# Optimization experiments

Hardware: AMD Instinct MI355X
Metric: run time of the kernel (lower is better)

The kernel has to match this reference:

```python
import jax, jax.numpy as jnp
import numpy as np

B, T, C = 64, 256, 384
H, D = 6, 64  # num_heads, head_size

def setup_inputs() -> dict:
    key = jax.random.key(0)
    ks = jax.random.split(key, 6)
    s = 0.02
    return {
        "x": jax.random.normal(ks[0], (B, T, C), dtype=jnp.float32),
        "Wq": jax.random.normal(ks[1], (H, C, D), dtype=jnp.float32) * s,
        "Wk": jax.random.normal(ks[2], (H, C, D), dtype=jnp.float32) * s,
        "Wv": jax.random.normal(ks[3], (H, C, D), dtype=jnp.float32) * s,
        "Wp": jax.random.normal(ks[4], (C, C), dtype=jnp.float32) * s,
        "bp": jnp.zeros((C,), dtype=jnp.float32),
    }

def reference(x, Wq, Wk, Wv, Wp, bp):
    # per-head projections: [B,T,C] x [H,C,D] -> [B,H,T,D]
    q = jnp.einsum('btc,hcd->bhtd', x, Wq)
    k = jnp.einsum('btc,hcd->bhtd', x, Wk)
    v = jnp.einsum('btc,hcd->bhtd', x, Wv)
    scale = 1.0 / jnp.sqrt(jnp.float32(D))
    scores = jnp.einsum('bhtd,bhsd->bhts', q, k) * scale  # [B,H,T,T]
    Tlen = x.shape[1]
    causal = jnp.tril(jnp.ones((Tlen, Tlen), dtype=bool))
    scores = jnp.where(causal, scores, -jnp.inf)
    wei = jax.nn.softmax(scores, axis=-1)
    # dropout is identity in eval mode
    out = jnp.einsum('bhts,bhsd->bhtd', wei, v)  # [B,H,T,D]
    # concat heads in order (matches torch.cat over head list)
    out = jnp.transpose(out, (0, 2, 1, 3)).reshape(x.shape[0], Tlen, H * D)
    return out @ Wp.T + bp  # nn.Linear: y = x W^T + b
```

## Files before the change

kernel.cpp:

```cpp
#include <hip/hip_runtime.h>

constexpr int Bn = 64, T = 256, C = 384, H = 6, D = 64;
constexpr int BT = Bn * T;
constexpr int NQKV = 3 * C;
constexpr int WALL_ELEMS = NQKV * C;
constexpr int WP_ELEMS = C * C;

using f32x4 = __attribute__((ext_vector_type(4))) float;
using fvec4 = __attribute__((ext_vector_type(4))) float;
using us8   = __attribute__((ext_vector_type(8))) unsigned short;
using bf8   = __attribute__((ext_vector_type(8))) __bf16;

__device__ __forceinline__ unsigned short f2bf(float f) {
  unsigned u = __builtin_bit_cast(unsigned, f);
  u += 0x7FFFu + ((u >> 16) & 1u);
  return (unsigned short)(u >> 16);
}

__device__ __forceinline__ f32x4 mfma16(us8 a, us8 b, f32x4 c) {
  return __builtin_amdgcn_mfma_f32_16x16x32_bf16(
      __builtin_bit_cast(bf8, a), __builtin_bit_cast(bf8, b), c, 0, 0, 0);
}

__global__ __launch_bounds__(256) void k_prep(
    const float* __restrict__ Wq, const float* __restrict__ Wk,
    const float* __restrict__ Wv, const float* __restrict__ Wp,
    unsigned short* __restrict__ Wall, unsigned short* __restrict__ Wpb) {
  int i = blockIdx.x * 256 + threadIdx.x;
  if (i < WALL_ELEMS) {
    int n = i / C, c = i % C;
    int p = n / C;
    int hd = n % C;
    int h = hd >> 6, d = hd & 63;
    const float* W = (p == 0) ? Wq : (p == 1) ? Wk : Wv;
    Wall[i] = f2bf(W[(h * C + c) * D + d]);
  } else {
    int j = i - WALL_ELEMS;
    if (j < WP_ELEMS) Wpb[j] = f2bf(Wp[j]);
  }
}

__global__ __launch_bounds__(256) void k_xcast(
    const float* __restrict__ x, unsigned short* __restrict__ Xb) {
  const int i = (blockIdx.x * 256 + threadIdx.x) * 8;
  fvec4 a = *(const fvec4*)(x + i);
  fvec4 b = *(const fvec4*)(x + i + 4);
  us8 o;
#pragma unroll
  for (int j = 0; j < 4; ++j) { o[j] = f2bf(a[j]); o[4 + j] = f2bf(b[j]); }
  *(us8*)(Xb + i) = o;
}

__device__ __forceinline__ void stage_tile(
    const unsigned short* __restrict__ g, unsigned short* l,
    int row0g, int k0, int tr, int tc, int w) {
#pragma unroll
  for (int s = 0; s < 4; ++s) {
    const int row = s * 32 + tr;
    const int sc = (tc ^ (row & 7)) * 8;
    const unsigned short* ga = g + (size_t)(row0g + row) * C + k0 + sc;
    unsigned short* la = l + (s * 32 + w * 8) * 64;
    __builtin_amdgcn_global_load_lds(
        (const __attribute__((address_space(1))) unsigned int*)ga,
        (__attribute__((address_space(3))) unsigned int*)la, 16, 0, 0);
  }
}

template <bool BF16_OUT>
__global__ __launch_bounds__(256) void k_gemm(
    const unsigned short* __restrict__ A,
    const unsigned short* __restrict__ Bm,
    const float* __restrict__ bias,
    unsigned short* __restrict__ Obf, float* __restrict__ Of, int Nld) {
  constexpr int BK = 64, NT = C / BK;
  __shared__ unsigned short Al[2][128 * BK];
  __shared__ unsigned short Bl[2][128 * BK];
  const int tid = threadIdx.x;
  const int w = tid >> 6, lane = tid & 63;
  const int lr = lane & 15, lg = lane >> 4;
  const int m0 = blockIdx.y * 128, n0 = blockIdx.x * 128;
  const int wm = (w >> 1) * 64, wn = (w & 1) * 64;
  const int tr = tid >> 3, tc = tid & 7;

  f32x4 acc[4][4];
#pragma unroll
  for (int i = 0; i < 4; ++i)
#pragma unroll
    for (int j = 0; j < 4; ++j) acc[i][j] = (f32x4){0.f, 0.f, 0.f, 0.f};

  stage_tile(A, &Al[0][0], m0, 0, tr, tc, w);
  stage_tile(Bm, &Bl[0][0], n0, 0, tr, tc, w);
  __syncthreads();

  int cur = 0;
  for (int t = 0; t < NT; ++t) {
    if (t + 1 < NT) {
      stage_tile(A, &Al[cur ^ 1][0], m0, (t + 1) * BK, tr, tc, w);
      stage_tile(Bm, &Bl[cur ^ 1][0], n0, (t + 1) * BK, tr, tc, w);
    }
#pragma unroll
    for (int kc = 0; kc < 2; ++kc) {
      us8 af[4], bfr[4];
#pragma unroll
      for (int i = 0; i < 4; ++i) {
        const int ra = wm + i * 16 + lr;
        af[i] = *(const us8*)&Al[cur][ra * 64 + (((kc * 4 + lg) ^ (ra & 7)) * 8)];
        const int rb = wn + i * 16 + lr;
        bfr[i] = *(const us8*)&Bl[cur][rb * 64 + (((kc * 4 + lg) ^ (rb & 7)) * 8)];
      }
#pragma unroll
      for (int i = 0; i < 4; ++i)
#pragma unroll
        for (int j = 0; j < 4; ++j)
          acc[i][j] = mfma16(af[i], bfr[j], acc[i][j]);
    }
    __syncthreads();
    cur ^= 1;
  }

#pragma unroll
  for (int i = 0; i < 4; ++i)
#pragma unroll
    for (int j = 0; j < 4; ++j) {
      const int col = n0 + wn + j * 16 + lr;
      float bv = BF16_OUT ? 0.f : bias[col];
#pragma unroll
      for (int r = 0; r < 4; ++r) {
        const size_t row = m0 + wm + i * 16 + lg * 4 + r;
        if (BF16_OUT)
          Obf[row * Nld + col] = f2bf(acc[i][j][r]);
        else
          Of[row * Nld + col] = acc[i][j][r] + bv;
      }
    }
}

__global__ __launch_bounds__(512) void k_attn(
    const unsigned short* __restrict__ QKV, unsigned short* __restrict__ Y) {
  __shared__ unsigned short Klds[256][72];
  __shared__ unsigned short Vt[64][264];
  __shared__ unsigned short Pch[8][16][40];
  const int qt = blockIdx.x, h = blockIdx.y, b = blockIdx.z;
  const int t0 = qt * 128;
  const int kvlen = t0 + 128;
  const int tid = threadIdx.x;
  const int w = tid >> 6, lane = tid & 63;
  const int lr = lane & 15, lg = lane >> 4;

  {
    const int c8 = (tid & 7) * 8;
    for (int r = tid >> 3; r < kvlen; r += 64) {
      const size_t base = (size_t)(b * T + r) * NQKV + h * D + c8;
      us8 kv = *(const us8*)(QKV + base + C);
      *(us8*)&Klds[r][c8] = kv;
      us8 vv = *(const us8*)(QKV + base + 2 * C);
#pragma unroll
      for (int j = 0; j < 8; ++j) Vt[c8 + j][r] = vv[j];
    }
  }
  __syncthreads();

  const size_t qbase = (size_t)(b * T + t0 + w * 16 + lr) * NQKV + h * D;
  const us8 aq0 = *(const us8*)(QKV + qbase + lg * 8);
  const us8 aq1 = *(const us8*)(QKV + qbase + 32 + lg * 8);

  const int nsf = kvlen / 16;

  f32x4 s[16];
#pragma unroll
  for (int sf = 0; sf < 16; ++sf) s[sf] = (f32x4){0.f, 0.f, 0.f, 0.f};
#pragma unroll
  for (int sf = 0; sf < 16; ++sf) {
    if (sf < nsf) {
      us8 kb0 = *(const us8*)&Klds[sf * 16 + lr][lg * 8];
      s[sf] = mfma16(aq0, kb0, s[sf]);
      us8 kb1 = *(const us8*)&Klds[sf * 16 + lr][32 + lg * 8];
      s[sf] = mfma16(aq1, kb1, s[sf]);
    }
  }

  float mrow[4] = {-1e30f, -1e30f, -1e30f, -1e30f};
#pragma unroll
  for (int sf = 0; sf < 16; ++sf) {
    if (sf < nsf) {
#pragma unroll
      for (int r = 0; r < 4; ++r) {
        const int trow = t0 + w * 16 + lg * 4 + r;
        const int scol = sf * 16 + lr;
        float v = s[sf][r] * 0.125f;
        if (scol > trow) v = -1e30f;
        s[sf][r] = v;
        mrow[r] = fmaxf(mrow[r], v);
      }
    }
  }
#pragma unroll
  for (int dd = 1; dd < 16; dd <<= 1)
#pragma unroll
    for (int r = 0; r < 4; ++r)
      mrow[r] = fmaxf(mrow[r], __shfl_xor(mrow[r], dd, 64));

  float psum[4] = {0.f, 0.f, 0.f, 0.f};
#pragma unroll
  for (int sf = 0; sf < 16; ++sf) {
    if (sf < nsf) {
#pragma unroll
      for (int r = 0; r < 4; ++r) {
        float p = __expf(s[sf][r] - mrow[r]);
        s[sf][r] = p;
        psum[r] += p;
      }
    }
  }
#pragma unroll
  for (int dd = 1; dd < 16; dd <<= 1)
#pragma unroll
    for (int r = 0; r < 4; ++r)
      psum[r] += __shfl_xor(psum[r], dd, 64);

  f32x4 o[4];
#pragma unroll
  for (int nf = 0; nf < 4; ++nf) o[nf] = (f32x4){0.f, 0.f, 0.f, 0.f};
  const int nkk = nsf >> 1;
#pragma unroll
  for (int kk = 0; kk < 8; ++kk) {
    if (kk < nkk) {
#pragma unroll
      for (int half = 0; half < 2; ++half) {
        const int sf = kk * 2 + half;
#pragma unroll
        for (int r = 0; r < 4; ++r)
          Pch[w][lg * 4 + r][half * 16 + lr] = f2bf(s[sf][r]);
      }
      __builtin_amdgcn_wave_barrier();
      us8 pa = *(const us8*)&Pch[w][lr][lg * 8];
      __builtin_amdgcn_wave_barrier();
#pragma unroll
      for (int nf = 0; nf < 4; ++nf) {
        us8 bv = *(const us8*)&Vt[nf * 16 + lr][kk * 32 + lg * 8];
        o[nf] = mfma16(pa, bv, o[nf]);
      }
    }
  }

  float rs[4];
#pragma unroll
  for (int r = 0; r < 4; ++r) rs[r] = 1.0f / psum[r];
#pragma unroll
  for (int nf = 0; nf < 4; ++nf)
#pragma unroll
    for (int r = 0; r < 4; ++r) {
      const int trow = t0 + w * 16 + lg * 4 + r;
      Y[(size_t)(b * T + trow) * C + h * D + nf * 16 + lr] =
          f2bf(o[nf][r] * rs[r]);
    }
}

extern "C" void kernel_launch(void* const* d_in, const int* in_sizes, int n_in,
                              void* d_out, int out_size, void* d_ws, size_t ws_size,
                              hipStream_t stream) {
  const float* x  = (const float*)d_in[0];
  const float* Wq = (const float*)d_in[1];
  const float* Wk = (const float*)d_in[2];
  const float* Wv = (const float*)d_in[3];
  const float* Wp = (const float*)d_in[4];
  const float* bp = (const float*)d_in[5];
  float* out = (float*)d_out;

  unsigned short* Wall = (unsigned short*)d_ws;
  unsigned short* Wpb  = Wall + WALL_ELEMS;
  unsigned short* QKV  = Wpb + WP_ELEMS;
  unsigned short* Yb   = QKV + (size_t)BT * NQKV;
  unsigned short* Xb   = Yb;

  k_prep<<<(WALL_ELEMS + WP_ELEMS) / 256, 256, 0, stream>>>(Wq, Wk, Wv, Wp,
                                                            Wall, Wpb);
  k_xcast<<<BT * C / (256 * 8), 256, 0, stream>>>(x, Xb);
  k_gemm<true><<<dim3(NQKV / 128, BT / 128), 256, 0, stream>>>(
      Xb, Wall, nullptr, QKV, nullptr, NQKV);
  k_attn<<<dim3(T / 128, H, Bn), 512, 0, stream>>>(QKV, Yb);
  k_gemm<false><<<dim3(C / 128, BT / 128), 256, 0, stream>>>(
      Yb, Wpb, bp, nullptr, out, C);
}
```

Before: 83.46 us.

## Transpose weights via LDS, remap blocks for XCD locality, swizzle P scratch

```diff
diff --git a/kernel.cpp b/kernel.cpp
--- a/kernel.cpp
+++ b/kernel.cpp
@@ -24,31 +24,47 @@
 
 __global__ __launch_bounds__(256) void k_prep(
     const float* __restrict__ Wq, const float* __restrict__ Wk,
-    const float* __restrict__ Wv, const float* __restrict__ Wp,
-    unsigned short* __restrict__ Wall, unsigned short* __restrict__ Wpb) {
-  int i = blockIdx.x * 256 + threadIdx.x;
-  if (i < WALL_ELEMS) {
-    int n = i / C, c = i % C;
-    int p = n / C;
-    int hd = n % C;
-    int h = hd >> 6, d = hd & 63;
-    const float* W = (p == 0) ? Wq : (p == 1) ? Wk : Wv;
-    Wall[i] = f2bf(W[(h * C + c) * D + d]);
-  } else {
-    int j = i - WALL_ELEMS;
-    if (j < WP_ELEMS) Wpb[j] = f2bf(Wp[j]);
+    const float* __restrict__ Wv, unsigned short* __restrict__ Wall) {
+  __shared__ unsigned short t[64][71];
+  const int bid = blockIdx.x;
+  const int ct = bid % 6, ph = bid / 6;
+  const int h = ph % 6, p = ph / 6;
+  const float* W = (p == 0) ? Wq : (p == 1) ? Wk : Wv;
+  const int c0 = ct * 64;
+  const int tid = threadIdx.x;
+  const int d = tid & 63, cq = tid >> 6;
+#pragma unroll
+  for (int s = 0; s < 16; ++s) {
+    const int c_loc = cq * 16 + s;
+    t[c_loc][d] = f2bf(W[(size_t)(h * C + c0 + c_loc) * D + d]);
+  }
+  __syncthreads();
+  const int d_loc = tid >> 2, ch = tid & 3;
+#pragma unroll
+  for (int it = 0; it < 2; ++it) {
+    const int cc = (ch + it * 4) * 8;
+    us8 o;
+#pragma unroll
+    for (int j = 0; j < 8; ++j) o[j] = t[cc + j][d_loc];
+    *(us8*)&Wall[(size_t)(p * C + h * D + d_loc) * C + c0 + cc] = o;
   }
 }
 
 __global__ __launch_bounds__(256) void k_xcast(
-    const float* __restrict__ x, unsigned short* __restrict__ Xb) {
+    const float* __restrict__ x, unsigned short* __restrict__ Xb,
+    const float* __restrict__ Wp, unsigned short* __restrict__ Wpb) {
   const int i = (blockIdx.x * 256 + threadIdx.x) * 8;
-  fvec4 a = *(const fvec4*)(x + i);
-  fvec4 b = *(const fvec4*)(x + i + 4);
+  const float* src;
+  unsigned short* dst;
+  int off;
+  if (i < BT * C) { src = x; dst = Xb; off = i; }
+  else { src = Wp; dst = Wpb; off = i - BT * C; }
+  fvec4 a = *(const fvec4*)(src + off);
+  fvec4 b = *(const fvec4*)(src + off + 4);
   us8 o;
 #pragma unroll
   for (int j = 0; j < 4; ++j) { o[j] = f2bf(a[j]); o[4 + j] = f2bf(b[j]); }
-  *(us8*)(Xb + i) = o;
+  *(us8*)(dst + off) = o;
 }
 
 __device__ __forceinline__ void stage_tile(
@@ -71,14 +87,18 @@
     const unsigned short* __restrict__ A,
     const unsigned short* __restrict__ Bm,
     const float* __restrict__ bias,
-    unsigned short* __restrict__ Obf, float* __restrict__ Of, int Nld) {
+    unsigned short* __restrict__ Obf, float* __restrict__ Of,
+    int Nld, int nwgn) {
   constexpr int BK = 64, NT = C / BK;
   __shared__ unsigned short Al[2][128 * BK];
   __shared__ unsigned short Bl[2][128 * BK];
+  const int nwg = gridDim.x;
+  const int bid = blockIdx.x;
+  const int lin = (bid & 7) * (nwg >> 3) + (bid >> 3);
+  const int m0 = (lin / nwgn) * 128, n0 = (lin % nwgn) * 128;
   const int tid = threadIdx.x;
   const int w = tid >> 6, lane = tid & 63;
   const int lr = lane & 15, lg = lane >> 4;
-  const int m0 = blockIdx.y * 128, n0 = blockIdx.x * 128;
   const int wm = (w >> 1) * 64, wn = (w & 1) * 64;
   const int tr = tid >> 3, tc = tid & 7;
 
@@ -135,12 +155,15 @@
     }
 }
 
-__global__ __launch_bounds__(512) void k_attn(
+__global__ __launch_bounds__(512, 4) void k_attn(
     const unsigned short* __restrict__ QKV, unsigned short* __restrict__ Y) {
   __shared__ unsigned short Klds[256][72];
   __shared__ unsigned short Vt[64][264];
-  __shared__ unsigned short Pch[8][16][40];
-  const int qt = blockIdx.x, h = blockIdx.y, b = blockIdx.z;
+  __shared__ unsigned short Pch[8][16][32];
+  const int bid = blockIdx.x;
+  const int lin = (bid & 7) * 96 + (bid >> 3);
+  const int b = lin / 12, rr = lin % 12;
+  const int h = rr >> 1, qt = rr & 1;
   const int t0 = qt * 128;
   const int kvlen = t0 + 128;
   const int tid = threadIdx.x;
@@ -228,12 +251,15 @@
 #pragma unroll
       for (int half = 0; half < 2; ++half) {
         const int sf = kk * 2 + half;
-#pragma unroll
-        for (int r = 0; r < 4; ++r)
-          Pch[w][lg * 4 + r][half * 16 + lr] = f2bf(s[sf][r]);
+        const int row = lg * 4;
+#pragma unroll
+        for (int r = 0; r < 4; ++r) {
+          const int cch = (half * 2 + (lr >> 3)) ^ ((row + r) & 3);
+          Pch[w][row + r][cch * 8 + (lr & 7)] = f2bf(s[sf][r]);
+        }
       }
       __builtin_amdgcn_wave_barrier();
-      us8 pa = *(const us8*)&Pch[w][lr][lg * 8];
+      us8 pa = *(const us8*)&Pch[w][lr][(lg ^ (lr & 3)) * 8];
       __builtin_amdgcn_wave_barrier();
 #pragma unroll
       for (int nf = 0; nf < 4; ++nf) {
@@ -273,12 +299,11 @@
   unsigned short* Yb   = QKV + (size_t)BT * NQKV;
   unsigned short* Xb   = Yb;
 
-  k_prep<<<(WALL_ELEMS + WP_ELEMS) / 256, 256, 0, stream>>>(Wq, Wk, Wv, Wp,
-                                                            Wall, Wpb);
-  k_xcast<<<BT * C / (256 * 8), 256, 0, stream>>>(x, Xb);
-  k_gemm<true><<<dim3(NQKV / 128, BT / 128), 256, 0, stream>>>(
-      Xb, Wall, nullptr, QKV, nullptr, NQKV);
-  k_attn<<<dim3(T / 128, H, Bn), 512, 0, stream>>>(QKV, Yb);
-  k_gemm<false><<<dim3(C / 128, BT / 128), 256, 0, stream>>>(
-      Yb, Wpb, bp, nullptr, out, C);
-}
+  k_prep<<<108, 256, 0, stream>>>(Wq, Wk, Wv, Wall);
+  k_xcast<<<(BT * C + WP_ELEMS) / (256 * 8), 256, 0, stream>>>(x, Xb, Wp, Wpb);
+  k_gemm<true><<<NQKV / 128 * (BT / 128), 256, 0, stream>>>(
+      Xb, Wall, nullptr, QKV, nullptr, NQKV, NQKV / 128);
+  k_attn<<<T / 128 * H * Bn, 512, 0, stream>>>(QKV, Yb);
+  k_gemm<false><<<C / 128 * (BT / 128), 256, 0, stream>>>(
+      Yb, Wpb, bp, nullptr, out, C, C / 128);
+}
```

Result: faster. 72.79 us (-12.8%).
